# Kernel optimization log

Hardware: AMD Instinct MI355X
Metric: run time of the kernel (lower is better)

## Reference

```python
import jax, jax.numpy as jnp
import numpy as np

NUM_CLASSES = 50000
K = 3
EMBED_DIM = 512
MARGIN = 0.5
SCALE = 30.0
EPS = 1e-7


def setup_inputs() -> dict:
    key = jax.random.key(0)
    k1, k2, k3 = jax.random.split(key, 3)
    B = 1024
    embeddings = jax.random.normal(k1, (B, EMBED_DIM), dtype=jnp.float32)
    labels = jax.random.randint(k2, (B,), 0, NUM_CLASSES)
    # xavier_normal-ish init scale
    std = (2.0 / (NUM_CLASSES * K + EMBED_DIM)) ** 0.5
    weight = jax.random.normal(k3, (NUM_CLASSES * K, EMBED_DIM), dtype=jnp.float32) * std
    return {"embeddings": embeddings, "labels": labels, "weight": weight}


def reference(embeddings, labels, weight):
    # L2-normalize embeddings and sub-center weights
    e = embeddings / jnp.linalg.norm(embeddings, axis=1, keepdims=True)  # [B, D]
    w = weight / jnp.linalg.norm(weight, axis=1, keepdims=True)          # [C*K, D]
    w = w.reshape(NUM_CLASSES, K, EMBED_DIM)                              # [C, K, D]
    # single batched matmul instead of per-class loop
    cos_all = jnp.einsum("bd,ckd->bck", e, w)                            # [B, C, K]
    cosine = jnp.max(cos_all, axis=2)                                     # [B, C]
    cosine = jnp.clip(cosine, -1.0 + EPS, 1.0 - EPS)
    theta = jnp.arccos(cosine)
    marginal = jnp.cos(theta + MARGIN)
    one_hot = jax.nn.one_hot(labels, NUM_CLASSES, dtype=cosine.dtype)     # [B, C]
    logits = SCALE * (one_hot * marginal + (1.0 - one_hot) * cosine)
    logp = jax.nn.log_softmax(logits, axis=1)
    loss = -jnp.mean(jnp.take_along_axis(logp, labels[:, None], axis=1))
    return loss
```

## Files before the change

kernel.cpp:

```cpp
#include <hip/hip_runtime.h>
#include <math.h>

typedef __attribute__((ext_vector_type(4))) float f32x4;
typedef __attribute__((ext_vector_type(8))) int  i32x8;

#define NCLS   50000
#define KSUB   3
#define DIM    512
#define NROWSW (NCLS*KSUB)
#define BQ     1024

#define SCALEF 30.0f
#define EPSC   1e-7f
#define COSM   0.8775825618903728f
#define SINM   0.4794255386042030f

#define BN     48
#define TW     3
#define NJ     2
#define NKQ    4
#define NTILES (NROWSW/BN)
#define NRG    128
#define NCG    4
#define TILEB  (BN*DIM)
#define SCL1   0x7F7F7F7F

__device__ __forceinline__ float wave_sum(float v) {
#pragma unroll
  for (int m = 1; m < 64; m <<= 1) v += __shfl_xor(v, m, 64);
  return v;
}

__device__ __forceinline__ unsigned pack4_fp8(float a, float b, float c, float d) {
  int v = 0;
  v = __builtin_amdgcn_cvt_pk_fp8_f32(a, b, v, false);
  v = __builtin_amdgcn_cvt_pk_fp8_f32(c, d, v, true);
  return (unsigned)v;
}

__device__ __forceinline__ float eterm(float v) {
  v = fminf(fmaxf(v, -1.f + EPSC), 1.f - EPSC);
  return __expf(SCALEF * v);
}

__global__ __launch_bounds__(256) void k_prenorm(const float* __restrict__ W,
                                                 unsigned char* __restrict__ Wn8) {
  const int row = blockIdx.x * 4 + (threadIdx.x >> 6);
  const int l = threadIdx.x & 63;
  const float4* p = reinterpret_cast<const float4*>(W + (size_t)row * DIM + l * 8);
  float4 a = p[0], d = p[1];
  float ss = a.x*a.x + a.y*a.y + a.z*a.z + a.w*a.w
           + d.x*d.x + d.y*d.y + d.z*d.z + d.w*d.w;
  ss = wave_sum(ss);
  float inv = rsqrtf(ss);
  uint2 o;
  o.x = pack4_fp8(a.x*inv, a.y*inv, a.z*inv, a.w*inv);
  o.y = pack4_fp8(d.x*inv, d.y*inv, d.z*inv, d.w*inv);
  *reinterpret_cast<uint2*>(Wn8 + (size_t)row * DIM + l * 8) = o;
}

__global__ __launch_bounds__(64) void k_prep(const float* __restrict__ E,
                                             const int* __restrict__ lab,
                                             const float* __restrict__ W,
                                             unsigned char* __restrict__ En8,
                                             float* __restrict__ delta,
                                             float* __restrict__ tl) {
  const int b = blockIdx.x, l = threadIdx.x;
  const float4* pe = reinterpret_cast<const float4*>(E + (size_t)b * DIM + l * 8);
  float4 e0 = pe[0], e1 = pe[1];
  float es = e0.x*e0.x + e0.y*e0.y + e0.z*e0.z + e0.w*e0.w
           + e1.x*e1.x + e1.y*e1.y + e1.z*e1.z + e1.w*e1.w;
  es = wave_sum(es);
  const float inv = rsqrtf(es);
  uint2 o;
  o.x = pack4_fp8(e0.x*inv, e0.y*inv, e0.z*inv, e0.w*inv);
  o.y = pack4_fp8(e1.x*inv, e1.y*inv, e1.z*inv, e1.w*inv);
  *reinterpret_cast<uint2*>(En8 + (size_t)b * DIM + l * 8) = o;

  const int L = lab[b];
  float mx = -2.f;
#pragma unroll
  for (int k = 0; k < KSUB; ++k) {
    const float4* pw = reinterpret_cast<const float4*>(W + (size_t)(L * KSUB + k) * DIM + l * 8);
    float4 w0 = pw[0], w1 = pw[1];
    float ds = e0.x*w0.x + e0.y*w0.y + e0.z*w0.z + e0.w*w0.w
             + e1.x*w1.x + e1.y*w1.y + e1.z*w1.z + e1.w*w1.w;
    float ws = w0.x*w0.x + w0.y*w0.y + w0.z*w0.z + w0.w*w0.w
             + w1.x*w1.x + w1.y*w1.y + w1.z*w1.z + w1.w*w1.w;
    ds = wave_sum(ds);
    ws = wave_sum(ws);
    float ck = ds * rsqrtf(es * ws);
    mx = fmaxf(mx, ck);
  }
  if (l == 0) {
    float cc = fminf(fmaxf(mx, -1.f + EPSC), 1.f - EPSC);
    float sn = sqrtf(fmaxf(1.f - cc * cc, 0.f));
    float mg = cc * COSM - sn * SINM;
    delta[b] = __expf(SCALEF * mg) - __expf(SCALEF * cc);
    tl[b]    = SCALEF * mg;
  }
}

__device__ __forceinline__ void stage_tile(const unsigned char* __restrict__ Wt,
                                           unsigned char* lbuf, int wv, int lane) {
#pragma unroll
  for (int i = 0; i < 3; ++i) {
    const int rlo = wv * 2 + (lane >> 5);
    const int r = i * 16 + rlo;
    const int m = (lane & 31) ^ rlo;
    const unsigned char* src = Wt + (size_t)r * DIM + m * 16;
    __builtin_amdgcn_global_load_lds(
        (const __attribute__((address_space(1))) unsigned int*)src,
        (__attribute__((address_space(3))) unsigned int*)(lbuf + (i * 16 + wv * 2) * DIM),
        16, 0, 0);
  }
}

__global__ __launch_bounds__(512, 4) void k_main(const unsigned char* __restrict__ Wn8,
                                                 const unsigned char* __restrict__ En8,
                                                 float* __restrict__ Zp) {
  __shared__ __align__(16) unsigned char wlds[2 * TILEB];
  const int tid  = threadIdx.x;
  const int lane = tid & 63;
  const int wv   = tid >> 6;
  const int g    = lane >> 4;
  const int c    = lane & 15;
  const int rg   = blockIdx.x & (NRG - 1);
  const int cg   = blockIdx.x >> 7;

  i32x8 bfr[NJ][NKQ];
#pragma unroll
  for (int j = 0; j < NJ; ++j) {
    const int col = cg * 256 + wv * 32 + j * 16 + c;
#pragma unroll
    for (int kq = 0; kq < NKQ; ++kq)
      bfr[j][kq] = *reinterpret_cast<const i32x8*>(
          En8 + (size_t)col * DIM + kq * 128 + g * 32);
  }

  float zreg[NJ];
#pragma unroll
  for (int j = 0; j < NJ; ++j) zreg[j] = 0.f;

  stage_tile(Wn8 + (size_t)rg * TILEB, wlds, wv, lane);
  __syncthreads();
  int cur = 0;

  for (int tile = rg; tile < NTILES; tile += NRG) {
    const int nxt = tile + NRG;
    if (nxt < NTILES)
      stage_tile(Wn8 + (size_t)nxt * TILEB, wlds + (cur ^ 1) * TILEB, wv, lane);

    const unsigned char* lbuf = wlds + cur * TILEB;

    f32x4 acc[TW][NJ];
#pragma unroll
    for (int t = 0; t < TW; ++t)
#pragma unroll
      for (int j = 0; j < NJ; ++j) acc[t][j] = (f32x4){0.f, 0.f, 0.f, 0.f};

#pragma unroll
    for (int kq = 0; kq < NKQ; ++kq) {
#pragma unroll
      for (int t = 0; t < TW; ++t) {
        const int r = t * 16 + c;
        const int s0 = (kq * 8 + 2 * g) ^ c;
        const int4 v0 = *reinterpret_cast<const int4*>(lbuf + r * DIM + s0 * 16);
        const int4 v1 = *reinterpret_cast<const int4*>(lbuf + r * DIM + (s0 ^ 1) * 16);
        i32x8 av;
        av[0] = v0.x; av[1] = v0.y; av[2] = v0.z; av[3] = v0.w;
        av[4] = v1.x; av[5] = v1.y; av[6] = v1.z; av[7] = v1.w;
#pragma unroll
        for (int j = 0; j < NJ; ++j)
          acc[t][j] = __builtin_amdgcn_mfma_scale_f32_16x16x128_f8f6f4(
              av, bfr[j][kq], acc[t][j], 0, 0, 0, SCL1, 0, SCL1);
      }
    }

#pragma unroll
    for (int j = 0; j < NJ; ++j) {
      float zc = 0.f;
#pragma unroll
      for (int t = 0; t < TW; ++t) {
        float s0, s1;
        if (t + 1 < TW) {
          s0 = (g == 0) ? acc[t + 1][j][0] : acc[t][j][0];
          s1 = (g == 0) ? acc[t + 1][j][1] : acc[t][j][1];
        } else {
          s0 = (g == 0) ? -2.f : acc[t][j][0];
          s1 = (g == 0) ? -2.f : acc[t][j][1];
        }
        float e0 = __shfl(s0, (lane + 16) & 63, 64);
        float e1 = __shfl(s1, (lane + 16) & 63, 64);
        const int m = (4 * t + g) % 3;
        float a0 = acc[t][j][0], a1 = acc[t][j][1], a2 = acc[t][j][2], a3 = acc[t][j][3];
        if (m == 0)      zc += eterm(fmaxf(fmaxf(a0, a1), a2)) + eterm(fmaxf(fmaxf(a3, e0), e1));
        else if (m == 1) zc += eterm(fmaxf(fmaxf(a2, a3), e0));
        else             zc += eterm(fmaxf(fmaxf(a1, a2), a3));
      }
      zreg[j] += zc;
    }

    __syncthreads();
    cur ^= 1;
  }

#pragma unroll
  for (int j = 0; j < NJ; ++j) {
    zreg[j] += __shfl_xor(zreg[j], 16, 64);
    zreg[j] += __shfl_xor(zreg[j], 32, 64);
  }
  if (g == 0) {
#pragma unroll
    for (int j = 0; j < NJ; ++j)
      Zp[(size_t)rg * BQ + cg * 256 + wv * 32 + j * 16 + c] = zreg[j];
  }
}

__global__ __launch_bounds__(256) void k_reduce(const float* __restrict__ Zp,
                                                const float* __restrict__ delta,
                                                const float* __restrict__ tl,
                                                float* __restrict__ part) {
  const int b = blockIdx.x * 256 + threadIdx.x;
  float z = 0.f;
#pragma unroll 8
  for (int nb = 0; nb < NRG; ++nb) z += Zp[(size_t)nb * BQ + b];
  float lossb = logf(z + delta[b]) - tl[b];
  __shared__ float sm[256];
  sm[threadIdx.x] = lossb;
  __syncthreads();
#pragma unroll
  for (int s = 128; s > 0; s >>= 1) {
    if (threadIdx.x < s) sm[threadIdx.x] += sm[threadIdx.x + s];
    __syncthreads();
  }
  if (threadIdx.x == 0) part[blockIdx.x] = sm[0];
}

__global__ void k_final(const float* __restrict__ part, float* __restrict__ out) {
  out[0] = (part[0] + part[1] + part[2] + part[3]) * (1.0f / BQ);
}

extern "C" void kernel_launch(void* const* d_in, const int* in_sizes, int n_in,
                              void* d_out, int out_size, void* d_ws, size_t ws_size,
                              hipStream_t stream) {
  const float* E  = (const float*)d_in[0];
  const int* lab  = (const int*)d_in[1];
  const float* W  = (const float*)d_in[2];

  char* ws = (char*)d_ws;
  unsigned char* En8 = (unsigned char*)ws;
  unsigned char* Wn8 = (unsigned char*)(ws + (size_t)BQ * DIM);
  char* after = ws + (size_t)BQ * DIM + (size_t)NROWSW * DIM;
  float* Zp    = (float*)after;
  float* delta = Zp + (size_t)NRG * BQ;
  float* tl    = delta + BQ;
  float* part  = tl + BQ;

  hipLaunchKernelGGL(k_prenorm, dim3(NROWSW / 4), dim3(256), 0, stream, W, Wn8);
  hipLaunchKernelGGL(k_prep,    dim3(BQ),         dim3(64),  0, stream, E, lab, W, En8, delta, tl);
  hipLaunchKernelGGL(k_main,    dim3(NRG * NCG),  dim3(512), 0, stream, Wn8, En8, Zp);
  hipLaunchKernelGGL(k_reduce,  dim3(4),          dim3(256), 0, stream, Zp, delta, tl, part);
  hipLaunchKernelGGL(k_final,   dim3(1),          dim3(1),   0, stream, part, (float*)d_out);
}
```

Baseline: 160.0 us.

## Fuse weight normalization and FP8 quantization into main GEMM tile staging

The prenorm kernel no longer writes an FP8 copy of the normalized weights. It now computes only per-row inverse norms. The main kernel reads the raw fp32 weights, scales them, packs them to FP8 and writes them into the swizzled LDS tile itself. This removes the FP8 weight write and its re-read. The cost is that each of the four column-group blocks re-reads fp32 weights, four times the bytes of the FP8 copy, and the asynchronous global-to-LDS copy becomes a register-staged synchronous load.

```diff
diff --git a/kernel.cpp b/kernel.cpp
--- a/kernel.cpp
+++ b/kernel.cpp
@@ -43,8 +43,8 @@
   return __expf(SCALEF * v);
 }
 
-__global__ __launch_bounds__(256) void k_prenorm(const float* __restrict__ W,
-                                                 unsigned char* __restrict__ Wn8) {
+__global__ __launch_bounds__(256) void k_rownorm(const float* __restrict__ W,
+                                                 float* __restrict__ invn) {
   const int row = blockIdx.x * 4 + (threadIdx.x >> 6);
   const int l = threadIdx.x & 63;
   const float4* p = reinterpret_cast<const float4*>(W + (size_t)row * DIM + l * 8);
@@ -52,11 +52,7 @@
   float ss = a.x*a.x + a.y*a.y + a.z*a.z + a.w*a.w
            + d.x*d.x + d.y*d.y + d.z*d.z + d.w*d.w;
   ss = wave_sum(ss);
-  float inv = rsqrtf(ss);
-  uint2 o;
-  o.x = pack4_fp8(a.x*inv, a.y*inv, a.z*inv, a.w*inv);
-  o.y = pack4_fp8(d.x*inv, d.y*inv, d.z*inv, d.w*inv);
-  *reinterpret_cast<uint2*>(Wn8 + (size_t)row * DIM + l * 8) = o;
+  if (l == 0) invn[row] = rsqrtf(ss);
 }
 
 __global__ __launch_bounds__(64) void k_prep(const float* __restrict__ E,
@@ -101,22 +97,25 @@
   }
 }
 
-__device__ __forceinline__ void stage_tile(const unsigned char* __restrict__ Wt,
-                                           unsigned char* lbuf, int wv, int lane) {
-#pragma unroll
-  for (int i = 0; i < 3; ++i) {
-    const int rlo = wv * 2 + (lane >> 5);
-    const int r = i * 16 + rlo;
-    const int m = (lane & 31) ^ rlo;
-    const unsigned char* src = Wt + (size_t)r * DIM + m * 16;
-    __builtin_amdgcn_global_load_lds(
-        (const __attribute__((address_space(1))) unsigned int*)src,
-        (__attribute__((address_space(3))) unsigned int*)(lbuf + (i * 16 + wv * 2) * DIM),
-        16, 0, 0);
-  }
-}
-
-__global__ __launch_bounds__(512, 4) void k_main(const unsigned char* __restrict__ Wn8,
+__device__ __forceinline__ void stage_tile_f32(const float* __restrict__ Wt,
+                                               const float* __restrict__ invt,
+                                               unsigned char* lbuf, int wv, int lane) {
+#pragma unroll 2
+  for (int i = 0; i < 6; ++i) {
+    const int r = wv * 6 + i;
+    const float inv = invt[r];
+    const float4* p = reinterpret_cast<const float4*>(Wt + (size_t)r * DIM + lane * 8);
+    float4 a = p[0], b = p[1];
+    uint2 o;
+    o.x = pack4_fp8(a.x*inv, a.y*inv, a.z*inv, a.w*inv);
+    o.y = pack4_fp8(b.x*inv, b.y*inv, b.z*inv, b.w*inv);
+    *reinterpret_cast<uint2*>(lbuf + r * DIM +
+                              (((lane >> 1) ^ (r & 15)) << 4) + (lane & 1) * 8) = o;
+  }
+}
+
+__global__ __launch_bounds__(512, 4) void k_main(const float* __restrict__ W,
+                                                 const float* __restrict__ invn,
                                                  const unsigned char* __restrict__ En8,
                                                  float* __restrict__ Zp) {
   __shared__ __align__(16) unsigned char wlds[2 * TILEB];
@@ -142,14 +141,15 @@
 #pragma unroll
   for (int j = 0; j < NJ; ++j) zreg[j] = 0.f;
 
-  stage_tile(Wn8 + (size_t)rg * TILEB, wlds, wv, lane);
+  stage_tile_f32(W + (size_t)rg * BN * DIM, invn + rg * BN, wlds, wv, lane);
   __syncthreads();
   int cur = 0;
 
   for (int tile = rg; tile < NTILES; tile += NRG) {
     const int nxt = tile + NRG;
     if (nxt < NTILES)
-      stage_tile(Wn8 + (size_t)nxt * TILEB, wlds + (cur ^ 1) * TILEB, wv, lane);
+      stage_tile_f32(W + (size_t)nxt * BN * DIM, invn + nxt * BN,
+                     wlds + (cur ^ 1) * TILEB, wv, lane);
 
     const unsigned char* lbuf = wlds + cur * TILEB;
 
@@ -250,16 +250,15 @@
 
   char* ws = (char*)d_ws;
   unsigned char* En8 = (unsigned char*)ws;
-  unsigned char* Wn8 = (unsigned char*)(ws + (size_t)BQ * DIM);
-  char* after = ws + (size_t)BQ * DIM + (size_t)NROWSW * DIM;
-  float* Zp    = (float*)after;
+  float* invn  = (float*)(ws + (size_t)BQ * DIM);
+  float* Zp    = invn + NROWSW;
   float* delta = Zp + (size_t)NRG * BQ;
   float* tl    = delta + BQ;
   float* part  = tl + BQ;
 
-  hipLaunchKernelGGL(k_prenorm, dim3(NROWSW / 4), dim3(256), 0, stream, W, Wn8);
+  hipLaunchKernelGGL(k_rownorm, dim3(NROWSW / 4), dim3(256), 0, stream, W, invn);
   hipLaunchKernelGGL(k_prep,    dim3(BQ),         dim3(64),  0, stream, E, lab, W, En8, delta, tl);
-  hipLaunchKernelGGL(k_main,    dim3(NRG * NCG),  dim3(512), 0, stream, Wn8, En8, Zp);
+  hipLaunchKernelGGL(k_main,    dim3(NRG * NCG),  dim3(512), 0, stream, W, invn, En8, Zp);
   hipLaunchKernelGGL(k_reduce,  dim3(4),          dim3(256), 0, stream, Zp, delta, tl, part);
   hipLaunchKernelGGL(k_final,   dim3(1),          dim3(1),   0, stream, part, (float*)d_out);
 }
```

New measurement: 209.3 us. 1.31x slower.

## Quantize normalized weights to MXFP4 with per-32 block scales for scaled MFMA

Applied to the files above, without the earlier changes.

The normalized weight matrix is now stored as FP4 (e2m1) with a shared power-of-two exponent per 32-element block, in place of FP8. The main kernel stages half as many bytes per tile into LDS and feeds the scaled MFMA with the A operand in FP4 format plus per-row block scales loaded from global memory. The aim is to halve weight bandwidth and LDS traffic in the dominant matmul. The cost is much coarser cosine precision, which may change the loss beyond tolerance, plus extra scale loads inside the inner loop.

```diff
diff --git a/kernel.cpp b/kernel.cpp
--- a/kernel.cpp
+++ b/kernel.cpp
@@ -22,7 +22,7 @@
 #define NTILES (NROWSW/BN)
 #define NRG    128
 #define NCG    4
-#define TILEB  (BN*DIM)
+#define TILE4B (BN*256)
 #define SCL1   0x7F7F7F7F
 
 __device__ __forceinline__ float wave_sum(float v) {
@@ -43,8 +43,24 @@
   return __expf(SCALEF * v);
 }
 
+__device__ __forceinline__ unsigned enc_e2m1(float x) {
+  unsigned s = (__float_as_uint(x) >> 31) << 3;
+  float v = fabsf(x);
+  unsigned m;
+  if      (v < 0.25f) m = 0;
+  else if (v < 0.75f) m = 1;
+  else if (v < 1.25f) m = 2;
+  else if (v < 1.75f) m = 3;
+  else if (v < 2.5f)  m = 4;
+  else if (v < 3.5f)  m = 5;
+  else if (v < 5.0f)  m = 6;
+  else                m = 7;
+  return s | m;
+}
+
 __global__ __launch_bounds__(256) void k_prenorm(const float* __restrict__ W,
-                                                 unsigned char* __restrict__ Wn8) {
+                                                 unsigned char* __restrict__ Wn4,
+                                                 unsigned* __restrict__ sigw) {
   const int row = blockIdx.x * 4 + (threadIdx.x >> 6);
   const int l = threadIdx.x & 63;
   const float4* p = reinterpret_cast<const float4*>(W + (size_t)row * DIM + l * 8);
@@ -52,11 +68,34 @@
   float ss = a.x*a.x + a.y*a.y + a.z*a.z + a.w*a.w
            + d.x*d.x + d.y*d.y + d.z*d.z + d.w*d.w;
   ss = wave_sum(ss);
-  float inv = rsqrtf(ss);
-  uint2 o;
-  o.x = pack4_fp8(a.x*inv, a.y*inv, a.z*inv, a.w*inv);
-  o.y = pack4_fp8(d.x*inv, d.y*inv, d.z*inv, d.w*inv);
-  *reinterpret_cast<uint2*>(Wn8 + (size_t)row * DIM + l * 8) = o;
+  const float inv = rsqrtf(ss);
+
+  float am = fmaxf(fmaxf(fmaxf(fabsf(a.x), fabsf(a.y)), fmaxf(fabsf(a.z), fabsf(a.w))),
+                   fmaxf(fmaxf(fabsf(d.x), fabsf(d.y)), fmaxf(fabsf(d.z), fabsf(d.w)))) * inv;
+  am = fmaxf(am, __shfl_xor(am, 1, 64));
+  am = fmaxf(am, __shfl_xor(am, 2, 64));
+
+  const float t6 = am * (1.0f / 6.0f);
+  const unsigned ut = __float_as_uint(t6);
+  int sg = (int)((ut >> 23) & 255) - 127 + ((ut & 0x7fffffu) ? 1 : 0);
+  if (!(am > 0.f)) sg = -100;
+  sg = sg < -100 ? -100 : (sg > 100 ? 100 : sg);
+  const float f = inv * __uint_as_float((unsigned)(127 - sg) << 23);
+
+  unsigned pk =  enc_e2m1(a.x * f)        | (enc_e2m1(a.y * f) << 4)
+              | (enc_e2m1(a.z * f) << 8)  | (enc_e2m1(a.w * f) << 12)
+              | (enc_e2m1(d.x * f) << 16) | (enc_e2m1(d.y * f) << 20)
+              | (enc_e2m1(d.z * f) << 24) | (enc_e2m1(d.w * f) << 28);
+  *reinterpret_cast<unsigned*>(Wn4 + (size_t)row * 256 + l * 4) = pk;
+
+  const unsigned bv = (unsigned)(127 + sg) & 0xffu;
+  const int base = l & 48;
+  const unsigned bA = __shfl(bv, base + 0, 64);
+  const unsigned bB = __shfl(bv, base + 4, 64);
+  const unsigned bC = __shfl(bv, base + 8, 64);
+  const unsigned bD = __shfl(bv, base + 12, 64);
+  if ((l & 15) == 0)
+    sigw[(size_t)row * 4 + (l >> 4)] = bA | (bB << 8) | (bC << 16) | (bD << 24);
 }
 
 __global__ __launch_bounds__(64) void k_prep(const float* __restrict__ E,
@@ -101,25 +140,31 @@
   }
 }
 
-__device__ __forceinline__ void stage_tile(const unsigned char* __restrict__ Wt,
-                                           unsigned char* lbuf, int wv, int lane) {
-#pragma unroll
-  for (int i = 0; i < 3; ++i) {
-    const int rlo = wv * 2 + (lane >> 5);
-    const int r = i * 16 + rlo;
-    const int m = (lane & 31) ^ rlo;
-    const unsigned char* src = Wt + (size_t)r * DIM + m * 16;
+__device__ __forceinline__ void stage4(const unsigned char* __restrict__ Wt,
+                                       unsigned char* lbuf, int wv, int lane) {
+  {
+    const int r = wv * 4 + (lane >> 4);
+    const int m = (lane & 15) ^ (r & 15);
     __builtin_amdgcn_global_load_lds(
-        (const __attribute__((address_space(1))) unsigned int*)src,
-        (__attribute__((address_space(3))) unsigned int*)(lbuf + (i * 16 + wv * 2) * DIM),
+        (const __attribute__((address_space(1))) unsigned int*)(Wt + (size_t)r * 256 + m * 16),
+        (__attribute__((address_space(3))) unsigned int*)(lbuf + wv * 1024),
         16, 0, 0);
   }
-}
-
-__global__ __launch_bounds__(512, 4) void k_main(const unsigned char* __restrict__ Wn8,
+  if (wv < 4) {
+    const int r = 32 + wv * 4 + (lane >> 4);
+    const int m = (lane & 15) ^ (r & 15);
+    __builtin_amdgcn_global_load_lds(
+        (const __attribute__((address_space(1))) unsigned int*)(Wt + (size_t)r * 256 + m * 16),
+        (__attribute__((address_space(3))) unsigned int*)(lbuf + (8 + wv) * 1024),
+        16, 0, 0);
+  }
+}
+
+__global__ __launch_bounds__(512, 4) void k_main(const unsigned char* __restrict__ Wn4,
+                                                 const unsigned* __restrict__ sigw,
                                                  const unsigned char* __restrict__ En8,
                                                  float* __restrict__ Zp) {
-  __shared__ __align__(16) unsigned char wlds[2 * TILEB];
+  __shared__ __align__(16) unsigned char wlds[2 * TILE4B];
   const int tid  = threadIdx.x;
   const int lane = tid & 63;
   const int wv   = tid >> 6;
@@ -142,16 +187,16 @@
 #pragma unroll
   for (int j = 0; j < NJ; ++j) zreg[j] = 0.f;
 
-  stage_tile(Wn8 + (size_t)rg * TILEB, wlds, wv, lane);
+  stage4(Wn4 + (size_t)rg * TILE4B, wlds, wv, lane);
   __syncthreads();
   int cur = 0;
 
   for (int tile = rg; tile < NTILES; tile += NRG) {
     const int nxt = tile + NRG;
     if (nxt < NTILES)
-      stage_tile(Wn8 + (size_t)nxt * TILEB, wlds + (cur ^ 1) * TILEB, wv, lane);
-
-    const unsigned char* lbuf = wlds + cur * TILEB;
+      stage4(Wn4 + (size_t)nxt * TILE4B, wlds + (cur ^ 1) * TILE4B, wv, lane);
+
+    const unsigned char* lbuf = wlds + cur * TILE4B;
 
     f32x4 acc[TW][NJ];
 #pragma unroll
@@ -164,16 +209,16 @@
 #pragma unroll
       for (int t = 0; t < TW; ++t) {
         const int r = t * 16 + c;
-        const int s0 = (kq * 8 + 2 * g) ^ c;
-        const int4 v0 = *reinterpret_cast<const int4*>(lbuf + r * DIM + s0 * 16);
-        const int4 v1 = *reinterpret_cast<const int4*>(lbuf + r * DIM + (s0 ^ 1) * 16);
-        i32x8 av;
-        av[0] = v0.x; av[1] = v0.y; av[2] = v0.z; av[3] = v0.w;
-        av[4] = v1.x; av[5] = v1.y; av[6] = v1.z; av[7] = v1.w;
+        const unsigned swd = sigw[(size_t)(tile * BN + r) * 4 + kq];
+        const unsigned sA = ((swd >> (g * 8)) & 0xffu) * 0x01010101u;
+        const int s = (kq * 4 + g) ^ c;
+        const int4 v = *reinterpret_cast<const int4*>(lbuf + r * 256 + s * 16);
+        i32x8 av = (i32x8){0, 0, 0, 0, 0, 0, 0, 0};
+        av[0] = v.x; av[1] = v.y; av[2] = v.z; av[3] = v.w;
 #pragma unroll
         for (int j = 0; j < NJ; ++j)
           acc[t][j] = __builtin_amdgcn_mfma_scale_f32_16x16x128_f8f6f4(
-              av, bfr[j][kq], acc[t][j], 0, 0, 0, SCL1, 0, SCL1);
+              av, bfr[j][kq], acc[t][j], 4, 0, 0, (int)sA, 0, SCL1);
       }
     }
 
@@ -250,16 +295,17 @@
 
   char* ws = (char*)d_ws;
   unsigned char* En8 = (unsigned char*)ws;
-  unsigned char* Wn8 = (unsigned char*)(ws + (size_t)BQ * DIM);
-  char* after = ws + (size_t)BQ * DIM + (size_t)NROWSW * DIM;
+  unsigned char* Wn4 = (unsigned char*)(ws + (size_t)BQ * DIM);
+  unsigned* sigw = (unsigned*)(ws + (size_t)BQ * DIM + (size_t)NROWSW * 256);
+  char* after = (char*)(sigw + (size_t)NROWSW * 4);
   float* Zp    = (float*)after;
   float* delta = Zp + (size_t)NRG * BQ;
   float* tl    = delta + BQ;
   float* part  = tl + BQ;
 
-  hipLaunchKernelGGL(k_prenorm, dim3(NROWSW / 4), dim3(256), 0, stream, W, Wn8);
+  hipLaunchKernelGGL(k_prenorm, dim3(NROWSW / 4), dim3(256), 0, stream, W, Wn4, sigw);
   hipLaunchKernelGGL(k_prep,    dim3(BQ),         dim3(64),  0, stream, E, lab, W, En8, delta, tl);
-  hipLaunchKernelGGL(k_main,    dim3(NRG * NCG),  dim3(512), 0, stream, Wn8, En8, Zp);
+  hipLaunchKernelGGL(k_main,    dim3(NRG * NCG),  dim3(512), 0, stream, Wn4, sigw, En8, Zp);
   hipLaunchKernelGGL(k_reduce,  dim3(4),          dim3(256), 0, stream, Zp, delta, tl, part);
   hipLaunchKernelGGL(k_final,   dim3(1),          dim3(1),   0, stream, part, (float*)d_out);
 }
```

New measurement: 228.8 us. 1.43x slower.
